# Optimization experiments

Hardware: AMD Instinct MI355X
Metric: run time of the kernel (lower is better)

## Reference

```python
import jax, jax.numpy as jnp
import numpy as np

B, T = 32768, 32
OBJ_V, PRED_V = 179, 46
E_OBJ, E_PRED, H = 5, 5, 32
IN_DIM = E_OBJ + E_PRED + 2 + 4  # 16, matches LSTMCell input size


def setup_inputs() -> dict:
    key = jax.random.key(0)
    ks = jax.random.split(key, 12)
    s = 0.1
    return {
        "input_objects": jax.random.randint(ks[0], (B, T), 0, OBJ_V),
        "input_boxes": jax.random.uniform(ks[1], (B, T, 4), dtype=jnp.float32),
        "predicates": jax.random.randint(ks[2], (B, T), 0, PRED_V),
        "subject_indicators": jax.random.randint(ks[3], (B, T), 0, 2),
        "target_object": jax.random.randint(ks[4], (B,), 0, OBJ_V),
        "obj_emb": jax.random.normal(ks[5], (OBJ_V, E_OBJ), dtype=jnp.float32) * s,
        "pred_emb": jax.random.normal(ks[6], (PRED_V, E_PRED), dtype=jnp.float32) * s,
        "W_ih": jax.random.normal(ks[7], (4 * H, IN_DIM), dtype=jnp.float32) * s,
        "W_hh": jax.random.normal(ks[8], (4 * H, H), dtype=jnp.float32) * s,
        "b_ih": jnp.zeros((4 * H,), dtype=jnp.float32),
        "b_hh": jnp.zeros((4 * H,), dtype=jnp.float32),
        "fc2_W": jax.random.normal(ks[9], (4, H), dtype=jnp.float32) * s,
        "fc2_b": jnp.zeros((4,), dtype=jnp.float32),
    }


def _forward(input_objects, input_boxes, predicates, subject_indicators,
             obj_emb, pred_emb, W_ih, W_hh, b_ih, b_hh, fc2_W, fc2_b):
    # concatenate_features, vectorized over all timesteps at once: [B,T,16]
    feats = jnp.concatenate([
        obj_emb[input_objects],                                   # [B,T,5]
        pred_emb[predicates],                                     # [B,T,5]
        jax.nn.one_hot(subject_indicators, 2, dtype=jnp.float32), # [B,T,2]
        input_boxes,                                              # [B,T,4]
    ], axis=-1)
    xs = jnp.transpose(feats, (1, 0, 2))  # [T,B,16] for scan over time

    def step(carry, x):
        h, c = carry
        gates = x @ W_ih.T + b_ih + h @ W_hh.T + b_hh  # [B,4H]
        i, f, g, o = jnp.split(gates, 4, axis=-1)      # torch gate order i,f,g,o
        i = jax.nn.sigmoid(i)
        f = jax.nn.sigmoid(f)
        g = jnp.tanh(g)
        o = jax.nn.sigmoid(o)
        c = f * c + i * g
        h = o * jnp.tanh(c)
        return (h, c), None

    h0 = jnp.zeros((input_objects.shape[0], H), dtype=jnp.float32)
    (h, _), _ = jax.lax.scan(step, (h0, h0), xs)
    out = h @ fc2_W.T + fc2_b          # output_fc2 on last hidden state
    return jnp.clip(out, 0.0, 1.0)     # torch.clamp(min=0, max=1)


def reference(input_objects, input_boxes, predicates, subject_indicators, target_object,
              obj_emb, pred_emb, W_ih, W_hh, b_ih, b_hh, fc2_W, fc2_b):
    # target_object is accepted by the torch forward but unused in its body
    return _forward(input_objects, input_boxes, predicates, subject_indicators,
                    obj_emb, pred_emb, W_ih, W_hh, b_ih, b_hh, fc2_W, fc2_b)
```

## Files before the change

### kernel.cpp

```cpp
#include <hip/hip_runtime.h>

#define LDS_BYTES 18720

typedef _Float16 f16x8 __attribute__((ext_vector_type(8)));
typedef __fp16   fp16x2 __attribute__((ext_vector_type(2)));
typedef float    f32x4 __attribute__((ext_vector_type(4)));
typedef float    f32x2 __attribute__((ext_vector_type(2)));

#define LOG2E     1.44269504088896f
#define TWO_LOG2E 2.88539008177793f

__global__ __launch_bounds__(256, 8)
void lstm_fused(const int* __restrict__ objs,
                const float* __restrict__ boxes,
                const int* __restrict__ preds,
                const int* __restrict__ subj,
                const float* __restrict__ obj_emb,
                const float* __restrict__ pred_emb,
                const float* __restrict__ W_ih,
                const float* __restrict__ W_hh,
                const float* __restrict__ b_ih,
                const float* __restrict__ b_hh,
                const float* __restrict__ fc2_W,
                const float* __restrict__ fc2_b,
                float* __restrict__ out)
{
    extern __shared__ char smem[];
    const int tid  = threadIdx.x;
    const int lane = tid & 63;
    const int wv   = tid >> 6;
    const int quad = lane >> 4;
    const int cidx = lane & 15;
    const int XOFF = 0, HX0 = 16640, HX1 = 17664, ZOFF = 18688;

    if (tid < 8) ((int*)(smem + ZOFF))[tid] = 0;

    {
        int b  = tid >> 4;
        int t0 = (tid & 15) << 1;
        long gb = (long)blockIdx.x * 16 + b;
        int2 ov = *(const int2*)(objs  + gb * 32 + t0);
        int2 pv = *(const int2*)(preds + gb * 32 + t0);
        int2 sv = *(const int2*)(subj  + gb * 32 + t0);
        int oarr[2] = {ov.x, ov.y};
        int parr[2] = {pv.x, pv.y};
        int sarr[2] = {sv.x, sv.y};
        #pragma unroll
        for (int tt = 0; tt < 2; ++tt) {
            int t = t0 + tt;
            const float* eo = obj_emb  + oarr[tt] * 5;
            const float* ep = pred_emb + parr[tt] * 5;
            float4 bx = *(const float4*)(boxes + (gb * 32 + t) * 4);
            f16x8 lo, hi;
            lo[0]=(_Float16)eo[0]; lo[1]=(_Float16)eo[1]; lo[2]=(_Float16)eo[2];
            lo[3]=(_Float16)eo[3]; lo[4]=(_Float16)eo[4];
            lo[5]=(_Float16)ep[0]; lo[6]=(_Float16)ep[1]; lo[7]=(_Float16)ep[2];
            hi[0]=(_Float16)ep[3]; hi[1]=(_Float16)ep[4];
            hi[2]=(_Float16)(sarr[tt]==0 ? 1.0f : 0.0f);
            hi[3]=(_Float16)(sarr[tt]==1 ? 1.0f : 0.0f);
            hi[4]=(_Float16)bx.x; hi[5]=(_Float16)bx.y;
            hi[6]=(_Float16)bx.z; hi[7]=(_Float16)bx.w;
            char* dst = smem + XOFF + b * 1040 + t * 32;
            *(f16x8*)dst        = lo;
            *(f16x8*)(dst + 16) = hi;
        }
    }

    f16x8 Wf[2][2];
    f32x4 bias4[2];
    #pragma unroll
    for (int tile = 0; tile < 2; ++tile) {
        int rm   = cidx & 3;
        int u    = 8 * (cidx >> 2) + 2 * wv + (rm & 1);
        int gate = tile * 2 + (rm >> 1);
        float scale = (gate == 2) ? TWO_LOG2E : -LOG2E;
        int n = gate * 32 + u;
        #pragma unroll
        for (int ks = 0; ks < 2; ++ks) {
            f16x8 v;
            #pragma unroll
            for (int jj = 0; jj < 8; ++jj) {
                int k = ks * 32 + quad * 8 + jj;
                float val = (k < 16) ? W_ih[n * 16 + k]
                          : (k >= 32) ? W_hh[n * 32 + (k - 32)]
                          : 0.0f;
                v[jj] = (_Float16)(val * scale);
            }
            Wf[tile][ks] = v;
        }
        #pragma unroll
        for (int r = 0; r < 4; ++r) {
            int ur = 8 * quad + 2 * wv + (r & 1);
            int gr = tile * 2 + (r >> 1);
            float sc = (gr == 2) ? TWO_LOG2E : -LOG2E;
            bias4[tile][r] = (b_ih[gr * 32 + ur] + b_hh[gr * 32 + ur]) * sc;
        }
    }

    const bool qlow = (quad < 2);
    int       xaddr = qlow ? (XOFF + cidx * 1040 + quad * 16) : ZOFF;
    const int xinc  = qlow ? 32 : 0;
    const int slot16 = lane << 4;
    const int wr_off = slot16 + (wv << 2);

    __syncthreads();

    f16x8 xfrag = *(const f16x8*)(smem + xaddr); xaddr += xinc;
    f32x4 accp[2];
    #pragma unroll
    for (int tile = 0; tile < 2; ++tile)
        accp[tile] = __builtin_amdgcn_mfma_f32_16x16x32_f16(Wf[tile][0], xfrag, bias4[tile], 0, 0, 0);

    union { int i[4]; f16x8 v; } hf;
    hf.i[0] = 0; hf.i[1] = 0; hf.i[2] = 0; hf.i[3] = 0;
    const f32x2 one = {1.0f, 1.0f};
    f32x2 cstv = {0.0f, 0.0f};
    f32x2 hv = {0.0f, 0.0f};

    #pragma unroll
    for (int t = 0; t < 32; ++t) {
        f32x4 acc0 = __builtin_amdgcn_mfma_f32_16x16x32_f16(Wf[0][1], hf.v, accp[0], 0, 0, 0);
        f32x4 acc1 = __builtin_amdgcn_mfma_f32_16x16x32_f16(Wf[1][1], hf.v, accp[1], 0, 0, 0);

        f16x8 xn = *(const f16x8*)(smem + xaddr); xaddr += xinc;

        f32x2 Ei = {__builtin_amdgcn_exp2f(acc0[0]), __builtin_amdgcn_exp2f(acc0[1])};
        f32x2 Ef = {__builtin_amdgcn_exp2f(acc0[2]), __builtin_amdgcn_exp2f(acc0[3])};
        f32x2 Eg = {__builtin_amdgcn_exp2f(acc1[0]), __builtin_amdgcn_exp2f(acc1[1])};
        f32x2 Eo = {__builtin_amdgcn_exp2f(acc1[2]), __builtin_amdgcn_exp2f(acc1[3])};

        f32x2 t1  = Ei + one;
        f32x2 dig = t1 * Eg + t1;
        f32x2 tf  = Ef + one;
        f32x2 nn  = (Eg - one) * tf + cstv * dig;
        f32x2 den = tf * dig;
        f32x2 rde = {__builtin_amdgcn_rcpf(den.x), __builtin_amdgcn_rcpf(den.y)};
        f32x2 c   = nn * rde;
        cstv = c;
        f32x2 cl  = c * TWO_LOG2E;
        f32x2 Ec  = {__builtin_amdgcn_exp2f(cl.x), __builtin_amdgcn_exp2f(cl.y)};
        f32x2 to  = Eo + one;
        f32x2 dh  = to * Ec + to;
        f32x2 rdh = {__builtin_amdgcn_rcpf(dh.x), __builtin_amdgcn_rcpf(dh.y)};
        hv = (Ec - one) * rdh;

        union { fp16x2 h; int i; } pku;
        pku.h = __builtin_amdgcn_cvt_pkrtz(hv.x, hv.y);

        char* buf = smem + ((t & 1) ? HX1 : HX0);
        *(int*)(buf + wr_off) = pku.i;
        __syncthreads();

        accp[0] = __builtin_amdgcn_mfma_f32_16x16x32_f16(Wf[0][0], xn, bias4[0], 0, 0, 0);
        accp[1] = __builtin_amdgcn_mfma_f32_16x16x32_f16(Wf[1][0], xn, bias4[1], 0, 0, 0);

        hf.v = *(const f16x8*)(buf + slot16);
    }

    __syncthreads();
    {
        int u0 = 8 * quad + 2 * wv;
        *(float2*)(smem + cidx * 144 + u0 * 4) = (float2){hv.x, hv.y};
    }
    __syncthreads();

    if (tid < 64) {
        int b = tid >> 2, jj = tid & 3;
        const float* fw   = fc2_W + jj * 32;
        const float* hrow = (const float*)(smem + b * 144);
        float s = fc2_b[jj];
        #pragma unroll
        for (int k = 0; k < 8; ++k) {
            float4 hvv = *(const float4*)(hrow + k * 4);
            s += fw[k*4+0] * hvv.x + fw[k*4+1] * hvv.y
               + fw[k*4+2] * hvv.z + fw[k*4+3] * hvv.w;
        }
        s = fminf(fmaxf(s, 0.0f), 1.0f);
        out[(long)blockIdx.x * 64 + tid] = s;
    }
}

extern "C" void kernel_launch(void* const* d_in, const int* in_sizes, int n_in,
                              void* d_out, int out_size, void* d_ws, size_t ws_size,
                              hipStream_t stream)
{
    lstm_fused<<<2048, 256, LDS_BYTES, stream>>>(
        (const int*)d_in[0], (const float*)d_in[1], (const int*)d_in[2],
        (const int*)d_in[3],
        (const float*)d_in[5], (const float*)d_in[6],
        (const float*)d_in[7], (const float*)d_in[8],
        (const float*)d_in[9], (const float*)d_in[10],
        (const float*)d_in[11], (const float*)d_in[12],
        (float*)d_out);
}
```

Measured before the change: 129.8 us.

## Process two independent batch chunks per block to interleave recurrent chains

Each block now handles 32 batch rows as two independent 16-row LSTM chains (A and B), issuing their MFMAs and gate math interleaved inside the same time loop. Both chains share one barrier per step. The goal is to hide MFMA and transcendental latency on the serial recurrence and to halve the barrier count per row. In exchange LDS per block doubles, the grid halves, launch bounds drop to 4 blocks per SM, the loop is unrolled only by 2, and register pressure rises.

```diff
diff --git a/kernel.cpp b/kernel.cpp
--- a/kernel.cpp
+++ b/kernel.cpp
@@ -1,6 +1,6 @@
 #include <hip/hip_runtime.h>
 
-#define LDS_BYTES 18720
+#define LDS_BYTES 37408
 
 typedef _Float16 f16x8 __attribute__((ext_vector_type(8)));
 typedef __fp16   fp16x2 __attribute__((ext_vector_type(2)));
@@ -10,7 +10,7 @@
 #define LOG2E     1.44269504088896f
 #define TWO_LOG2E 2.88539008177793f
 
-__global__ __launch_bounds__(256, 8)
+__global__ __launch_bounds__(256, 4)
 void lstm_fused(const int* __restrict__ objs,
                 const float* __restrict__ boxes,
                 const int* __restrict__ preds,
@@ -31,22 +31,23 @@
     const int wv   = tid >> 6;
     const int quad = lane >> 4;
     const int cidx = lane & 15;
-    const int XOFF = 0, HX0 = 16640, HX1 = 17664, ZOFF = 18688;
+    const int HXB = 33280, ZOFF = 37376;
 
     if (tid < 8) ((int*)(smem + ZOFF))[tid] = 0;
 
     {
-        int b  = tid >> 4;
-        int t0 = (tid & 15) << 1;
-        long gb = (long)blockIdx.x * 16 + b;
-        int2 ov = *(const int2*)(objs  + gb * 32 + t0);
-        int2 pv = *(const int2*)(preds + gb * 32 + t0);
-        int2 sv = *(const int2*)(subj  + gb * 32 + t0);
-        int oarr[2] = {ov.x, ov.y};
-        int parr[2] = {pv.x, pv.y};
-        int sarr[2] = {sv.x, sv.y};
-        #pragma unroll
-        for (int tt = 0; tt < 2; ++tt) {
+        int row = tid >> 3;
+        int t0  = (tid & 7) << 2;
+        long gb = (long)blockIdx.x * 32 + row;
+        int4 ov = *(const int4*)(objs  + gb * 32 + t0);
+        int4 pv = *(const int4*)(preds + gb * 32 + t0);
+        int4 sv = *(const int4*)(subj  + gb * 32 + t0);
+        int oarr[4] = {ov.x, ov.y, ov.z, ov.w};
+        int parr[4] = {pv.x, pv.y, pv.z, pv.w};
+        int sarr[4] = {sv.x, sv.y, sv.z, sv.w};
+        char* base = smem + row * 1040;
+        #pragma unroll
+        for (int tt = 0; tt < 4; ++tt) {
             int t = t0 + tt;
             const float* eo = obj_emb  + oarr[tt] * 5;
             const float* ep = pred_emb + parr[tt] * 5;
@@ -60,7 +61,7 @@
             hi[3]=(_Float16)(sarr[tt]==1 ? 1.0f : 0.0f);
             hi[4]=(_Float16)bx.x; hi[5]=(_Float16)bx.y;
             hi[6]=(_Float16)bx.z; hi[7]=(_Float16)bx.w;
-            char* dst = smem + XOFF + b * 1040 + t * 32;
+            char* dst = base + t * 32;
             *(f16x8*)dst        = lo;
             *(f16x8*)(dst + 16) = hi;
         }
@@ -98,76 +99,117 @@
     }
 
     const bool qlow = (quad < 2);
-    int       xaddr = qlow ? (XOFF + cidx * 1040 + quad * 16) : ZOFF;
-    const int xinc  = qlow ? 32 : 0;
+    int xaddrA = qlow ? (0     + cidx * 1040 + quad * 16) : ZOFF;
+    int xaddrB = qlow ? (16640 + cidx * 1040 + quad * 16) : ZOFF;
+    const int xinc   = qlow ? 32 : 0;
     const int slot16 = lane << 4;
     const int wr_off = slot16 + (wv << 2);
 
     __syncthreads();
 
-    f16x8 xfrag = *(const f16x8*)(smem + xaddr); xaddr += xinc;
-    f32x4 accp[2];
-    #pragma unroll
-    for (int tile = 0; tile < 2; ++tile)
-        accp[tile] = __builtin_amdgcn_mfma_f32_16x16x32_f16(Wf[tile][0], xfrag, bias4[tile], 0, 0, 0);
-
-    union { int i[4]; f16x8 v; } hf;
-    hf.i[0] = 0; hf.i[1] = 0; hf.i[2] = 0; hf.i[3] = 0;
+    f32x4 accpA[2], accpB[2];
+    {
+        f16x8 xfA = *(const f16x8*)(smem + xaddrA); xaddrA += xinc;
+        f16x8 xfB = *(const f16x8*)(smem + xaddrB); xaddrB += xinc;
+        #pragma unroll
+        for (int tile = 0; tile < 2; ++tile) {
+            accpA[tile] = __builtin_amdgcn_mfma_f32_16x16x32_f16(Wf[tile][0], xfA, bias4[tile], 0, 0, 0);
+            accpB[tile] = __builtin_amdgcn_mfma_f32_16x16x32_f16(Wf[tile][0], xfB, bias4[tile], 0, 0, 0);
+        }
+    }
+
+    union { int i[4]; f16x8 v; } hfA, hfB;
+    hfA.i[0]=0; hfA.i[1]=0; hfA.i[2]=0; hfA.i[3]=0;
+    hfB.i[0]=0; hfB.i[1]=0; hfB.i[2]=0; hfB.i[3]=0;
     const f32x2 one = {1.0f, 1.0f};
-    f32x2 cstv = {0.0f, 0.0f};
-    f32x2 hv = {0.0f, 0.0f};
-
-    #pragma unroll
+    f32x2 cstA = {0.0f, 0.0f}, cstB = {0.0f, 0.0f};
+    f32x2 hvA = {0.0f, 0.0f}, hvB = {0.0f, 0.0f};
+
+    #pragma unroll 2
     for (int t = 0; t < 32; ++t) {
-        f32x4 acc0 = __builtin_amdgcn_mfma_f32_16x16x32_f16(Wf[0][1], hf.v, accp[0], 0, 0, 0);
-        f32x4 acc1 = __builtin_amdgcn_mfma_f32_16x16x32_f16(Wf[1][1], hf.v, accp[1], 0, 0, 0);
-
-        f16x8 xn = *(const f16x8*)(smem + xaddr); xaddr += xinc;
-
-        f32x2 Ei = {__builtin_amdgcn_exp2f(acc0[0]), __builtin_amdgcn_exp2f(acc0[1])};
-        f32x2 Ef = {__builtin_amdgcn_exp2f(acc0[2]), __builtin_amdgcn_exp2f(acc0[3])};
-        f32x2 Eg = {__builtin_amdgcn_exp2f(acc1[0]), __builtin_amdgcn_exp2f(acc1[1])};
-        f32x2 Eo = {__builtin_amdgcn_exp2f(acc1[2]), __builtin_amdgcn_exp2f(acc1[3])};
-
-        f32x2 t1  = Ei + one;
-        f32x2 dig = t1 * Eg + t1;
-        f32x2 tf  = Ef + one;
-        f32x2 nn  = (Eg - one) * tf + cstv * dig;
-        f32x2 den = tf * dig;
-        f32x2 rde = {__builtin_amdgcn_rcpf(den.x), __builtin_amdgcn_rcpf(den.y)};
-        f32x2 c   = nn * rde;
-        cstv = c;
-        f32x2 cl  = c * TWO_LOG2E;
-        f32x2 Ec  = {__builtin_amdgcn_exp2f(cl.x), __builtin_amdgcn_exp2f(cl.y)};
-        f32x2 to  = Eo + one;
-        f32x2 dh  = to * Ec + to;
-        f32x2 rdh = {__builtin_amdgcn_rcpf(dh.x), __builtin_amdgcn_rcpf(dh.y)};
-        hv = (Ec - one) * rdh;
-
-        union { fp16x2 h; int i; } pku;
-        pku.h = __builtin_amdgcn_cvt_pkrtz(hv.x, hv.y);
-
-        char* buf = smem + ((t & 1) ? HX1 : HX0);
-        *(int*)(buf + wr_off) = pku.i;
+        f32x4 aA0 = __builtin_amdgcn_mfma_f32_16x16x32_f16(Wf[0][1], hfA.v, accpA[0], 0, 0, 0);
+        f32x4 aA1 = __builtin_amdgcn_mfma_f32_16x16x32_f16(Wf[1][1], hfA.v, accpA[1], 0, 0, 0);
+        f32x4 aB0 = __builtin_amdgcn_mfma_f32_16x16x32_f16(Wf[0][1], hfB.v, accpB[0], 0, 0, 0);
+        f32x4 aB1 = __builtin_amdgcn_mfma_f32_16x16x32_f16(Wf[1][1], hfB.v, accpB[1], 0, 0, 0);
+
+        f16x8 xnA = *(const f16x8*)(smem + xaddrA); xaddrA += xinc;
+        f16x8 xnB = *(const f16x8*)(smem + xaddrB); xaddrB += xinc;
+
+        int pkA, pkB;
+        {
+            f32x2 Ei = {__builtin_amdgcn_exp2f(aA0[0]), __builtin_amdgcn_exp2f(aA0[1])};
+            f32x2 Ef = {__builtin_amdgcn_exp2f(aA0[2]), __builtin_amdgcn_exp2f(aA0[3])};
+            f32x2 Eg = {__builtin_amdgcn_exp2f(aA1[0]), __builtin_amdgcn_exp2f(aA1[1])};
+            f32x2 Eo = {__builtin_amdgcn_exp2f(aA1[2]), __builtin_amdgcn_exp2f(aA1[3])};
+            f32x2 t1  = Ei + one;
+            f32x2 dig = t1 * Eg + t1;
+            f32x2 tf  = Ef + one;
+            f32x2 nn  = (Eg - one) * tf + cstA * dig;
+            f32x2 den = tf * dig;
+            f32x2 rde = {__builtin_amdgcn_rcpf(den.x), __builtin_amdgcn_rcpf(den.y)};
+            f32x2 c   = nn * rde;
+            cstA = c;
+            f32x2 cl  = c * TWO_LOG2E;
+            f32x2 Ec  = {__builtin_amdgcn_exp2f(cl.x), __builtin_amdgcn_exp2f(cl.y)};
+            f32x2 to  = Eo + one;
+            f32x2 dh  = to * Ec + to;
+            f32x2 rdh = {__builtin_amdgcn_rcpf(dh.x), __builtin_amdgcn_rcpf(dh.y)};
+            hvA = (Ec - one) * rdh;
+            union { fp16x2 h; int i; } pku;
+            pku.h = __builtin_amdgcn_cvt_pkrtz(hvA.x, hvA.y);
+            pkA = pku.i;
+        }
+        {
+            f32x2 Ei = {__builtin_amdgcn_exp2f(aB0[0]), __builtin_amdgcn_exp2f(aB0[1])};
+            f32x2 Ef = {__builtin_amdgcn_exp2f(aB0[2]), __builtin_amdgcn_exp2f(aB0[3])};
+            f32x2 Eg = {__builtin_amdgcn_exp2f(aB1[0]), __builtin_amdgcn_exp2f(aB1[1])};
+            f32x2 Eo = {__builtin_amdgcn_exp2f(aB1[2]), __builtin_amdgcn_exp2f(aB1[3])};
+            f32x2 t1  = Ei + one;
+            f32x2 dig = t1 * Eg + t1;
+            f32x2 tf  = Ef + one;
+            f32x2 nn  = (Eg - one) * tf + cstB * dig;
+            f32x2 den = tf * dig;
+            f32x2 rde = {__builtin_amdgcn_rcpf(den.x), __builtin_amdgcn_rcpf(den.y)};
+            f32x2 c   = nn * rde;
+            cstB = c;
+            f32x2 cl  = c * TWO_LOG2E;
+            f32x2 Ec  = {__builtin_amdgcn_exp2f(cl.x), __builtin_amdgcn_exp2f(cl.y)};
+            f32x2 to  = Eo + one;
+            f32x2 dh  = to * Ec + to;
+            f32x2 rdh = {__builtin_amdgcn_rcpf(dh.x), __builtin_amdgcn_rcpf(dh.y)};
+            hvB = (Ec - one) * rdh;
+            union { fp16x2 h; int i; } pku;
+            pku.h = __builtin_amdgcn_cvt_pkrtz(hvB.x, hvB.y);
+            pkB = pku.i;
+        }
+
+        char* buf = smem + HXB + ((t & 1) ? 2048 : 0);
+        *(int*)(buf + wr_off)        = pkA;
+        *(int*)(buf + 1024 + wr_off) = pkB;
         __syncthreads();
 
-        accp[0] = __builtin_amdgcn_mfma_f32_16x16x32_f16(Wf[0][0], xn, bias4[0], 0, 0, 0);
-        accp[1] = __builtin_amdgcn_mfma_f32_16x16x32_f16(Wf[1][0], xn, bias4[1], 0, 0, 0);
-
-        hf.v = *(const f16x8*)(buf + slot16);
+        accpA[0] = __builtin_amdgcn_mfma_f32_16x16x32_f16(Wf[0][0], xnA, bias4[0], 0, 0, 0);
+        accpA[1] = __builtin_amdgcn_mfma_f32_16x16x32_f16(Wf[1][0], xnA, bias4[1], 0, 0, 0);
+        accpB[0] = __builtin_amdgcn_mfma_f32_16x16x32_f16(Wf[0][0], xnB, bias4[0], 0, 0, 0);
+        accpB[1] = __builtin_amdgcn_mfma_f32_16x16x32_f16(Wf[1][0], xnB, bias4[1], 0, 0, 0);
+
+        hfA.v = *(const f16x8*)(buf + slot16);
+        hfB.v = *(const f16x8*)(buf + 1024 + slot16);
     }
 
     __syncthreads();
     {
         int u0 = 8 * quad + 2 * wv;
-        *(float2*)(smem + cidx * 144 + u0 * 4) = (float2){hv.x, hv.y};
+        *(float2*)(smem +        cidx * 144 + u0 * 4) = (float2){hvA.x, hvA.y};
+        *(float2*)(smem + 2304 + cidx * 144 + u0 * 4) = (float2){hvB.x, hvB.y};
     }
     __syncthreads();
 
-    if (tid < 64) {
-        int b = tid >> 2, jj = tid & 3;
+    if (tid < 128) {
+        int ch = tid >> 6, sub = tid & 63;
+        int b = sub >> 2, jj = sub & 3;
         const float* fw   = fc2_W + jj * 32;
-        const float* hrow = (const float*)(smem + b * 144);
+        const float* hrow = (const float*)(smem + ch * 2304 + b * 144);
         float s = fc2_b[jj];
         #pragma unroll
         for (int k = 0; k < 8; ++k) {
@@ -176,7 +218,7 @@
                + fw[k*4+2] * hvv.z + fw[k*4+3] * hvv.w;
         }
         s = fminf(fmaxf(s, 0.0f), 1.0f);
-        out[(long)blockIdx.x * 64 + tid] = s;
+        out[(long)blockIdx.x * 128 + tid] = s;
     }
 }
 
@@ -184,7 +226,7 @@
                               void* d_out, int out_size, void* d_ws, size_t ws_size,
                               hipStream_t stream)
 {
-    lstm_fused<<<2048, 256, LDS_BYTES, stream>>>(
+    lstm_fused<<<1024, 256, LDS_BYTES, stream>>>(
         (const int*)d_in[0], (const float*)d_in[1], (const int*)d_in[2],
         (const int*)d_in[3],
         (const float*)d_in[5], (const float*)d_in[6],
```

Result: no change. 130.2 us (+0.4%).
